# Kernel tuning notes

Measured on AMD Instinct MI355X. Metric: run time of the kernel, lower is better.

Reference implementation:

```python
import jax, jax.numpy as jnp
import numpy as np

HEAD_DIM = 128
N_HEADS = 64
N_KV = 8
N_REP = 8
DIM = 5120
HID = 25600
EPS_LN = 1e-5
EPS_QK = 1e-6
MAX_SEQ = 1024
BSZ = 32


def rmsnorm(x, w, eps):
    xf = x.astype(jnp.float32)
    n = xf * jax.lax.rsqrt(jnp.mean(xf * xf, axis=-1, keepdims=True) + eps)
    return n.astype(x.dtype) * w


def rope(x, cos, sin):
    # x: [b, s, h, d]; cos/sin: [s, d//2]. Complex rotation on (even, odd) pairs.
    xr = x[..., 0::2]
    xi = x[..., 1::2]
    c = cos[None, :, None, :]
    s = sin[None, :, None, :]
    o_r = xr * c - xi * s
    o_i = xr * s + xi * c
    return jnp.stack([o_r, o_i], axis=-1).reshape(x.shape)


def setup_inputs() -> dict:
    key = jax.random.key(0)
    ks = jax.random.split(key, 12)
    seqlen = 1
    start_pos = MAX_SEQ - seqlen
    x = jax.random.normal(ks[0], (BSZ, seqlen, DIM), jnp.float32)
    pos = np.arange(start_pos, start_pos + seqlen)
    inv = 1.0 / (10000.0 ** (np.arange(0, HEAD_DIM, 2, dtype=np.float64) / HEAD_DIM))
    ang = pos[:, None] * inv[None, :]
    freqs_cos = jnp.asarray(np.cos(ang), jnp.float32)
    freqs_sin = jnp.asarray(np.sin(ang), jnp.float32)
    mask = jnp.zeros((1, 1, seqlen, start_pos + seqlen), jnp.float32)
    cache_k = jax.random.normal(ks[1], (BSZ, MAX_SEQ, N_KV, HEAD_DIM), jnp.float32)
    cache_v = jax.random.normal(ks[2], (BSZ, MAX_SEQ, N_KV, HEAD_DIM), jnp.float32)
    s = 0.02
    wq = jax.random.normal(ks[3], (N_HEADS * HEAD_DIM, DIM), jnp.float32) * s
    wk = jax.random.normal(ks[4], (N_KV * HEAD_DIM, DIM), jnp.float32) * s
    wv = jax.random.normal(ks[5], (N_KV * HEAD_DIM, DIM), jnp.float32) * s
    wo = jax.random.normal(ks[6], (DIM, N_HEADS * HEAD_DIM), jnp.float32) * s
    w1 = jax.random.normal(ks[7], (HID, DIM), jnp.float32) * s
    w2 = jax.random.normal(ks[8], (DIM, HID), jnp.float32) * s
    w3 = jax.random.normal(ks[9], (HID, DIM), jnp.float32) * s
    attn_norm_w = jnp.ones((DIM,), jnp.float32)
    ffn_norm_w = jnp.ones((DIM,), jnp.float32)
    q_norm_w = jnp.ones((HEAD_DIM,), jnp.float32)
    k_norm_w = jnp.ones((HEAD_DIM,), jnp.float32)
    return dict(x=x, start_pos=start_pos, freqs_cos=freqs_cos, freqs_sin=freqs_sin,
                mask=mask, cache_k=cache_k, cache_v=cache_v,
                wq=wq, wk=wk, wv=wv, wo=wo, w1=w1, w2=w2, w3=w3,
                attn_norm_w=attn_norm_w, ffn_norm_w=ffn_norm_w,
                q_norm_w=q_norm_w, k_norm_w=k_norm_w)


def reference(x, start_pos, freqs_cos, freqs_sin, mask, cache_k, cache_v,
              wq, wk, wv, wo, w1, w2, w3,
              attn_norm_w, ffn_norm_w, q_norm_w, k_norm_w):
    bsz, seqlen, _ = x.shape
    # --- attention branch ---
    an = rmsnorm(x, attn_norm_w, EPS_LN)
    xq = (an @ wq.T).reshape(bsz, seqlen, N_HEADS, HEAD_DIM)
    xk = (an @ wk.T).reshape(bsz, seqlen, N_KV, HEAD_DIM)
    xv = (an @ wv.T).reshape(bsz, seqlen, N_KV, HEAD_DIM)
    xq = rmsnorm(xq, q_norm_w, EPS_QK)
    xk = rmsnorm(xk, k_norm_w, EPS_QK)
    xq = rope(xq, freqs_cos, freqs_sin)
    xk = rope(xk, freqs_cos, freqs_sin)
    # KV-cache write (start_pos is a static Python int)
    cache_k = cache_k.at[:bsz, start_pos:start_pos + seqlen].set(xk)
    cache_v = cache_v.at[:bsz, start_pos:start_pos + seqlen].set(xv)
    L = start_pos + seqlen
    keys = cache_k[:bsz, :L]      # [b, L, g, d]
    values = cache_v[:bsz, :L]    # [b, L, g, d]
    # GQA via grouped einsum (math-equivalent to repeat_kv then matmul)
    qg = xq.reshape(bsz, seqlen, N_KV, N_REP, HEAD_DIM)  # head = g*N_REP + r
    scores = jnp.einsum('bqgrd,blgd->bgrql', qg, keys) / np.sqrt(HEAD_DIM).astype(np.float32)
    scores = scores + mask[:, :, None, :, :]  # [1,1,1,q,L] broadcast
    probs = jax.nn.softmax(scores.astype(jnp.float32), axis=-1).astype(xq.dtype)
    attn = jnp.einsum('bgrql,blgd->bqgrd', probs, values)
    attn = attn.reshape(bsz, seqlen, N_HEADS * HEAD_DIM)
    h = x + attn @ wo.T
    # --- SwiGLU FFN branch ---
    fn = rmsnorm(h, ffn_norm_w, EPS_LN)
    ff = (jax.nn.silu(fn @ w1.T) * (fn @ w3.T)) @ w2.T
    return h + ff
```

## Files before the change

kernel.cpp:

```cpp
#include <hip/hip_runtime.h>
#include <math.h>

#define DIM   5120
#define QD    8192
#define KVD   1024
#define NQKV  10240
#define NH    64
#define NKV   8
#define HD    128
#define HID   25600
#define SEQL  1024
#define BSZ   32
#define NSEG  8

typedef __attribute__((ext_vector_type(8))) short short8;
typedef __attribute__((ext_vector_type(4))) float f32x4;
typedef __attribute__((ext_vector_type(4))) unsigned short us4;

__device__ __forceinline__ unsigned short f2bf(float f) {
  unsigned u = __builtin_bit_cast(unsigned, f);
  unsigned r = u + 0x7fffu + ((u >> 16) & 1u);
  return (unsigned short)(r >> 16);
}
__device__ __forceinline__ float bf2f(unsigned short b) {
  return __builtin_bit_cast(float, (unsigned)b << 16);
}
__device__ __forceinline__ unsigned cvt2(float lo, float hi) {
  unsigned r;
  asm("v_cvt_pk_bf16_f32 %0, %1, %2" : "=v"(r) : "v"(lo), "v"(hi));
  return r;
}
__device__ __forceinline__ short8 cvt8(float4 a, float4 b) {
  union { unsigned u[4]; short8 s; } o;
  o.u[0] = cvt2(a.x, a.y);
  o.u[1] = cvt2(a.z, a.w);
  o.u[2] = cvt2(b.x, b.y);
  o.u[3] = cvt2(b.z, b.w);
  return o.s;
}
__device__ __forceinline__ float fma4(float4 a, float4 b, float acc) {
  acc = fmaf(a.x, b.x, acc);
  acc = fmaf(a.y, b.y, acc);
  acc = fmaf(a.z, b.z, acc);
  acc = fmaf(a.w, b.w, acc);
  return acc;
}

__global__ __launch_bounds__(256) void rmsnorm_bf_kernel(
    const float* __restrict__ x, const float* __restrict__ w,
    unsigned short* __restrict__ out, float eps) {
  int b = blockIdx.x, t = threadIdx.x;
  const float4* xp = reinterpret_cast<const float4*>(x + (size_t)b * DIM);
  const float4* wp = reinterpret_cast<const float4*>(w);
  us4* op = reinterpret_cast<us4*>(out + (size_t)b * DIM);
  float4 v[5];
  float ss = 0.f;
#pragma unroll
  for (int j = 0; j < 5; ++j) {
    v[j] = xp[t + j * 256];
    ss = fma4(v[j], v[j], ss);
  }
#pragma unroll
  for (int m = 1; m < 64; m <<= 1) ss += __shfl_xor(ss, m);
  __shared__ float red[4];
  if ((t & 63) == 0) red[t >> 6] = ss;
  __syncthreads();
  float sc = rsqrtf((red[0] + red[1] + red[2] + red[3]) * (1.f / DIM) + eps);
#pragma unroll
  for (int j = 0; j < 5; ++j) {
    float4 wv = wp[t + j * 256];
    us4 o;
    o[0] = f2bf(v[j].x * sc * wv.x);
    o[1] = f2bf(v[j].y * sc * wv.y);
    o[2] = f2bf(v[j].z * sc * wv.z);
    o[3] = f2bf(v[j].w * sc * wv.w);
    op[t + j * 256] = o;
  }
}

template <int OUT_BF>
__device__ __forceinline__ void gemm_body(
    const unsigned short* __restrict__ Abf, const float* __restrict__ W,
    void* __restrict__ outp, int K, int k0, int kLen,
    int n0row, int n0col, int Nstride, int t) {
  const int wid = t >> 6, lane = t & 63;
  const int r = lane & 15, kg = lane >> 4;
  const float* wp = W + (size_t)(n0row + wid * 16 + r) * K + k0 + kg * 8;
  const unsigned short* ap0 = Abf + (size_t)r * K + k0 + kg * 8;
  const unsigned short* ap1 = ap0 + (size_t)16 * K;
  f32x4 acc0 = {0.f, 0.f, 0.f, 0.f}, acc1 = {0.f, 0.f, 0.f, 0.f};
#pragma unroll 2
  for (int kk = 0; kk < kLen; kk += 64) {
    float4 w00 = *reinterpret_cast<const float4*>(wp);
    float4 w01 = *reinterpret_cast<const float4*>(wp + 4);
    float4 w10 = *reinterpret_cast<const float4*>(wp + 32);
    float4 w11 = *reinterpret_cast<const float4*>(wp + 36);
    short8 a00 = *reinterpret_cast<const short8*>(ap0);
    short8 a01 = *reinterpret_cast<const short8*>(ap0 + 32);
    short8 a10 = *reinterpret_cast<const short8*>(ap1);
    short8 a11 = *reinterpret_cast<const short8*>(ap1 + 32);
    short8 wf0 = cvt8(w00, w01);
    short8 wf1 = cvt8(w10, w11);
    acc0 = __builtin_amdgcn_mfma_f32_16x16x32_bf16(wf0, a00, acc0, 0, 0, 0);
    acc1 = __builtin_amdgcn_mfma_f32_16x16x32_bf16(wf0, a10, acc1, 0, 0, 0);
    acc0 = __builtin_amdgcn_mfma_f32_16x16x32_bf16(wf1, a01, acc0, 0, 0, 0);
    acc1 = __builtin_amdgcn_mfma_f32_16x16x32_bf16(wf1, a11, acc1, 0, 0, 0);
    wp += 64; ap0 += 64; ap1 += 64;
  }
  int ncol = n0col + wid * 16 + kg * 4;
#pragma unroll
  for (int j = 0; j < 4; ++j) {
    if (OUT_BF) {
      unsigned short* o = (unsigned short*)outp;
      o[(size_t)r * Nstride + ncol + j] = f2bf(acc0[j]);
      o[(size_t)(r + 16) * Nstride + ncol + j] = f2bf(acc1[j]);
    } else {
      float* o = (float*)outp;
      o[(size_t)r * Nstride + ncol + j] = acc0[j];
      o[(size_t)(r + 16) * Nstride + ncol + j] = acc1[j];
    }
  }
}

__global__ __launch_bounds__(128) void qkv_gemm_kernel(
    const unsigned short* __restrict__ an_bf, const float* __restrict__ wq,
    const float* __restrict__ wk, const float* __restrict__ wv,
    float* __restrict__ part) {
  int n = blockIdx.x * 32;
  const float* W;
  int n0row;
  if (n < QD)            { W = wq; n0row = n; }
  else if (n < QD + KVD) { W = wk; n0row = n - QD; }
  else                   { W = wv; n0row = n - QD - KVD; }
  float* outp = part + (size_t)blockIdx.y * BSZ * NQKV;
  gemm_body<0>(an_bf, W, outp, DIM, blockIdx.y * 1280, 1280, n0row, n, NQKV,
               threadIdx.x);
}

__global__ __launch_bounds__(128) void wo_gemm_kernel(
    const unsigned short* __restrict__ ao_bf, const float* __restrict__ wo,
    float* __restrict__ part) {
  int n = blockIdx.x * 32;
  float* outp = part + (size_t)blockIdx.y * BSZ * DIM;
  gemm_body<0>(ao_bf, wo, outp, QD, blockIdx.y * 1024, 1024, n, n, DIM,
               threadIdx.x);
}

__global__ __launch_bounds__(128) void w13_gemm_kernel(
    const unsigned short* __restrict__ fn_bf, const float* __restrict__ w1,
    const float* __restrict__ w3, unsigned short* __restrict__ g13) {
  int n = blockIdx.x * 32;
  const float* W;
  int n0row;
  if (n < HID) { W = w1; n0row = n; }
  else         { W = w3; n0row = n - HID; }
  gemm_body<1>(fn_bf, W, g13, DIM, 0, DIM, n0row, n, 2 * HID, threadIdx.x);
}

__global__ __launch_bounds__(128) void w2_gemm_kernel(
    const unsigned short* __restrict__ gg_bf, const float* __restrict__ w2,
    float* __restrict__ part) {
  int n = blockIdx.x * 32;
  float* outp = part + (size_t)blockIdx.y * BSZ * DIM;
  gemm_body<0>(gg_bf, w2, outp, HID, blockIdx.y * 3200, 3200, n, n, DIM,
               threadIdx.x);
}

__global__ __launch_bounds__(64) void qkv_finish_kernel(
    const float* __restrict__ part, const float* __restrict__ qw,
    const float* __restrict__ kw, const float* __restrict__ fcos,
    const float* __restrict__ fsin, float* __restrict__ xqkv) {
  int h = blockIdx.x, b = blockIdx.y, j = threadIdx.x;
  int base;
  const float* w = nullptr;
  int dorope = 1;
  if (h < NH)            { base = h * HD; w = qw; }
  else if (h < NH + NKV) { base = QD + (h - NH) * HD; w = kw; }
  else                   { base = QD + KVD + (h - NH - NKV) * HD; dorope = 0; }
  size_t off = (size_t)b * NQKV + base;
  float s0 = 0.f, s1 = 0.f;
#pragma unroll
  for (int g = 0; g < 4; ++g) {
    const float* p = part + (size_t)g * BSZ * NQKV + off;
    s0 += p[2 * j];
    s1 += p[2 * j + 1];
  }
  if (dorope) {
    float ss = s0 * s0 + s1 * s1;
#pragma unroll
    for (int m = 1; m < 64; m <<= 1) ss += __shfl_xor(ss, m);
    float sc = rsqrtf(ss * (1.f / HD) + 1e-6f);
    float n0 = s0 * sc * w[2 * j];
    float n1 = s1 * sc * w[2 * j + 1];
    float c = fcos[j], s = fsin[j];
    xqkv[off + 2 * j]     = n0 * c - n1 * s;
    xqkv[off + 2 * j + 1] = n0 * s + n1 * c;
  } else {
    xqkv[off + 2 * j]     = s0;
    xqkv[off + 2 * j + 1] = s1;
  }
}

__global__ __launch_bounds__(256) void wo_finish_kernel(
    const float* __restrict__ part, const float* __restrict__ x,
    const float* __restrict__ fw, float* __restrict__ h,
    unsigned short* __restrict__ fn_bf, float eps) {
  int b = blockIdx.x, t = threadIdx.x;
  const float4* xp = reinterpret_cast<const float4*>(x + (size_t)b * DIM);
  const float4* wp = reinterpret_cast<const float4*>(fw);
  float4* hp = reinterpret_cast<float4*>(h + (size_t)b * DIM);
  us4* fp = reinterpret_cast<us4*>(fn_bf + (size_t)b * DIM);
  float4 v[5];
  float ss = 0.f;
#pragma unroll
  for (int j = 0; j < 5; ++j) {
    int idx = t + j * 256;
    float4 s = xp[idx];
#pragma unroll
    for (int g = 0; g < 8; ++g) {
      float4 p = reinterpret_cast<const float4*>(
          part + (size_t)g * BSZ * DIM + (size_t)b * DIM)[idx];
      s.x += p.x; s.y += p.y; s.z += p.z; s.w += p.w;
    }
    v[j] = s;
    ss = fma4(s, s, ss);
    hp[idx] = s;
  }
#pragma unroll
  for (int m = 1; m < 64; m <<= 1) ss += __shfl_xor(ss, m);
  __shared__ float red[4];
  if ((t & 63) == 0) red[t >> 6] = ss;
  __syncthreads();
  float sc = rsqrtf((red[0] + red[1] + red[2] + red[3]) * (1.f / DIM) + eps);
#pragma unroll
  for (int j = 0; j < 5; ++j) {
    float4 wv = wp[t + j * 256];
    us4 o;
    o[0] = f2bf(v[j].x * sc * wv.x);
    o[1] = f2bf(v[j].y * sc * wv.y);
    o[2] = f2bf(v[j].z * sc * wv.z);
    o[3] = f2bf(v[j].w * sc * wv.w);
    fp[t + j * 256] = o;
  }
}

template <int SEGS>
__global__ __launch_bounds__(256) void combine_kernel(
    const float* __restrict__ part, const float* __restrict__ resid,
    float* __restrict__ out, int total) {
  int i = blockIdx.x * 256 + threadIdx.x;
  if (i >= total) return;
  float s = 0.f;
#pragma unroll
  for (int g = 0; g < SEGS; ++g) s += part[(size_t)g * total + i];
  if (resid) s += resid[i];
  out[i] = s;
}

__global__ __launch_bounds__(256) void attn_kernel(
    const float* __restrict__ xqkv, const float* __restrict__ ck,
    const float* __restrict__ cv, float* __restrict__ pacc,
    float* __restrict__ pml) {
  int g = blockIdx.x, b = blockIdx.y, z = blockIdx.z, t = threadIdx.x;
  __shared__ float qs[8][128];
  __shared__ float tk[128][33];
  __shared__ float tv[32][132];
  __shared__ float st[8][32];
  __shared__ float m_s[8], sum_s[8], fac_s[8];
  const float* qbase = xqkv + (size_t)b * NQKV;
  for (int i = t; i < 8 * 128; i += 256)
    qs[i >> 7][i & 127] = qbase[(g * 8 + (i >> 7)) * HD + (i & 127)];
  if (t < 8) { m_s[t] = -1e30f; sum_s[t] = 0.f; }
  int r = t >> 5, d5 = t & 31;
  float4 acc = make_float4(0.f, 0.f, 0.f, 0.f);
  for (int ti = 0; ti < 1024 / NSEG / 32; ++ti) {
    int l0 = z * (1024 / NSEG) + ti * 32;
    __syncthreads();
#pragma unroll
    for (int jj = 0; jj < 4; ++jj) {
      int i = t + jj * 256;
      int l = i >> 5, d4 = i & 31;
      int gl = l0 + l;
      float4 kv, vv;
      if (gl == 1023) {
        kv = *reinterpret_cast<const float4*>(qbase + QD + g * HD + d4 * 4);
        vv = *reinterpret_cast<const float4*>(qbase + QD + KVD + g * HD + d4 * 4);
      } else {
        size_t base = (((size_t)b * SEQL + gl) * NKV + g) * HD + d4 * 4;
        kv = *reinterpret_cast<const float4*>(ck + base);
        vv = *reinterpret_cast<const float4*>(cv + base);
      }
      tk[d4 * 4 + 0][l] = kv.x;
      tk[d4 * 4 + 1][l] = kv.y;
      tk[d4 * 4 + 2][l] = kv.z;
      tk[d4 * 4 + 3][l] = kv.w;
      *reinterpret_cast<float4*>(&tv[l][d4 * 4]) = vv;
    }
    __syncthreads();
    {
      int l = t & 31, rr = t >> 5;
      float s = 0.f;
#pragma unroll 8
      for (int d = 0; d < 128; ++d) s = fmaf(qs[rr][d], tk[d][l], s);
      st[rr][l] = s * 0.08838834764831845f;
    }
    __syncthreads();
    {
      float sv = st[r][d5];
      float tm = sv;
#pragma unroll
      for (int m = 1; m < 32; m <<= 1) tm = fmaxf(tm, __shfl_xor(tm, m));
      float mo = m_s[r];
      float mn = fmaxf(mo, tm);
      float fac = __expf(mo - mn);
      float e = __expf(sv - mn);
      st[r][d5] = e;
      float ps = e;
#pragma unroll
      for (int m = 1; m < 32; m <<= 1) ps += __shfl_xor(ps, m);
      if (d5 == 0) {
        sum_s[r] = sum_s[r] * fac + ps;
        m_s[r] = mn;
        fac_s[r] = fac;
      }
    }
    __syncthreads();
    {
      float fac = fac_s[r];
      acc.x *= fac; acc.y *= fac; acc.z *= fac; acc.w *= fac;
#pragma unroll 4
      for (int l = 0; l < 32; ++l) {
        float p = st[r][l];
        float4 vv = *reinterpret_cast<const float4*>(&tv[l][d5 * 4]);
        acc.x = fmaf(p, vv.x, acc.x);
        acc.y = fmaf(p, vv.y, acc.y);
        acc.z = fmaf(p, vv.z, acc.z);
        acc.w = fmaf(p, vv.w, acc.w);
      }
    }
  }
  size_t idx = ((size_t)b * NH + g * 8 + r) * NSEG + z;
  *reinterpret_cast<float4*>(pacc + idx * HD + d5 * 4) = acc;
  if (d5 == 0) {
    pml[idx * 2]     = m_s[r];
    pml[idx * 2 + 1] = sum_s[r];
  }
}

__global__ __launch_bounds__(128) void attn_combine_kernel(
    const float* __restrict__ pacc, const float* __restrict__ pml,
    unsigned short* __restrict__ ao_bf) {
  int h = blockIdx.x, b = blockIdx.y, d = threadIdx.x;
  size_t base = ((size_t)b * NH + h) * NSEG;
  float M = -1e30f;
#pragma unroll
  for (int s = 0; s < NSEG; ++s) M = fmaxf(M, pml[(base + s) * 2]);
  float L = 0.f, o = 0.f;
#pragma unroll
  for (int s = 0; s < NSEG; ++s) {
    float w = __expf(pml[(base + s) * 2] - M);
    L += pml[(base + s) * 2 + 1] * w;
    o += pacc[(base + s) * HD + d] * w;
  }
  ao_bf[((size_t)b * NH + h) * HD + d] = f2bf(o / L);
}

__global__ __launch_bounds__(256) void silu_mul_bf_kernel(
    const unsigned short* __restrict__ g13, unsigned short* __restrict__ gg) {
  int j = blockIdx.x * 256 + threadIdx.x;
  int b = blockIdx.y;
  float a = bf2f(g13[(size_t)b * 2 * HID + j]);
  float c = bf2f(g13[(size_t)b * 2 * HID + HID + j]);
  gg[(size_t)b * HID + j] = f2bf((a / (1.f + __expf(-a))) * c);
}

extern "C" void kernel_launch(void* const* d_in, const int* in_sizes, int n_in,
                              void* d_out, int out_size, void* d_ws, size_t ws_size,
                              hipStream_t stream) {
  const float* x    = (const float*)d_in[0];
  const float* fcos = (const float*)d_in[2];
  const float* fsin = (const float*)d_in[3];
  const float* ck   = (const float*)d_in[5];
  const float* cv   = (const float*)d_in[6];
  const float* wq   = (const float*)d_in[7];
  const float* wk   = (const float*)d_in[8];
  const float* wv   = (const float*)d_in[9];
  const float* wo   = (const float*)d_in[10];
  const float* w1   = (const float*)d_in[11];
  const float* w2   = (const float*)d_in[12];
  const float* w3   = (const float*)d_in[13];
  const float* anw  = (const float*)d_in[14];
  const float* fnw  = (const float*)d_in[15];
  const float* qnw  = (const float*)d_in[16];
  const float* knw  = (const float*)d_in[17];
  float* out = (float*)d_out;

  char* wsb = (char*)d_ws;
  float* scratch = (float*)wsb;                 wsb += 16 * 1024 * 1024;
  unsigned short* an_bf  = (unsigned short*)wsb; wsb += (size_t)BSZ * DIM * 2;
  unsigned short* ao_bf  = (unsigned short*)wsb; wsb += (size_t)BSZ * QD * 2;
  unsigned short* g13_bf = (unsigned short*)wsb; wsb += (size_t)BSZ * 2 * HID * 2;
  unsigned short* gg_bf  = (unsigned short*)wsb; wsb += (size_t)BSZ * HID * 2;
  unsigned short* fn_bf  = (unsigned short*)wsb; wsb += (size_t)BSZ * DIM * 2;
  float*          xqkv   = (float*)wsb;          wsb += (size_t)BSZ * NQKV * 4;
  float*          h      = (float*)wsb;          wsb += (size_t)BSZ * DIM * 4;
  float* pacc = scratch;
  float* pml  = scratch + (size_t)BSZ * NH * NSEG * HD;

  rmsnorm_bf_kernel<<<BSZ, 256, 0, stream>>>(x, anw, an_bf, 1e-5f);
  qkv_gemm_kernel<<<dim3(NQKV / 32, 4), 128, 0, stream>>>(an_bf, wq, wk, wv, scratch);
  qkv_finish_kernel<<<dim3(NH + 2 * NKV, BSZ), 64, 0, stream>>>(
      scratch, qnw, knw, fcos, fsin, xqkv);
  attn_kernel<<<dim3(NKV, BSZ, NSEG), 256, 0, stream>>>(xqkv, ck, cv, pacc, pml);
  attn_combine_kernel<<<dim3(NH, BSZ), 128, 0, stream>>>(pacc, pml, ao_bf);
  wo_gemm_kernel<<<dim3(DIM / 32, 8), 128, 0, stream>>>(ao_bf, wo, scratch);
  wo_finish_kernel<<<BSZ, 256, 0, stream>>>(scratch, x, fnw, h, fn_bf, 1e-5f);
  w13_gemm_kernel<<<dim3(2 * HID / 32, 1), 128, 0, stream>>>(fn_bf, w1, w3, g13_bf);
  silu_mul_bf_kernel<<<dim3(HID / 256, BSZ), 256, 0, stream>>>(g13_bf, gg_bf);
  w2_gemm_kernel<<<dim3(DIM / 32, 8), 128, 0, stream>>>(gg_bf, w2, scratch);
  combine_kernel<8><<<(BSZ * DIM + 255) / 256, 256, 0, stream>>>(
      scratch, h, out, BSZ * DIM);
}
```

Before: 658.9 us.

## Stage weight tiles through LDS with coalesced prefetched loads in GEMMs

Rewrites the shared GEMM body so a 256-thread block cooperatively loads a 32-row by 128-column fp32 weight tile with coalesced float4 reads. It converts the tile to bf16 into padded LDS and prefetches the next tile into registers. Each of four waves then computes one 16x16 output tile from LDS-resident weights and global activations. The aim is better DRAM access patterns for the weight-streaming GEMMs, at the cost of two block barriers per k-step and fewer outstanding loads per thread.

```diff
diff --git a/kernel.cpp b/kernel.cpp
--- a/kernel.cpp
+++ b/kernel.cpp
@@ -25,19 +25,6 @@
 __device__ __forceinline__ float bf2f(unsigned short b) {
   return __builtin_bit_cast(float, (unsigned)b << 16);
 }
-__device__ __forceinline__ unsigned cvt2(float lo, float hi) {
-  unsigned r;
-  asm("v_cvt_pk_bf16_f32 %0, %1, %2" : "=v"(r) : "v"(lo), "v"(hi));
-  return r;
-}
-__device__ __forceinline__ short8 cvt8(float4 a, float4 b) {
-  union { unsigned u[4]; short8 s; } o;
-  o.u[0] = cvt2(a.x, a.y);
-  o.u[1] = cvt2(a.z, a.w);
-  o.u[2] = cvt2(b.x, b.y);
-  o.u[3] = cvt2(b.z, b.w);
-  return o.s;
-}
 __device__ __forceinline__ float fma4(float4 a, float4 b, float acc) {
   acc = fmaf(a.x, b.x, acc);
   acc = fmaf(a.y, b.y, acc);
@@ -78,51 +65,68 @@
   }
 }
 
+#define LDSW 136
 template <int OUT_BF>
 __device__ __forceinline__ void gemm_body(
     const unsigned short* __restrict__ Abf, const float* __restrict__ W,
     void* __restrict__ outp, int K, int k0, int kLen,
     int n0row, int n0col, int Nstride, int t) {
-  const int wid = t >> 6, lane = t & 63;
+  __shared__ unsigned short lw[32 * LDSW];
+  const int lane = t & 63;
   const int r = lane & 15, kg = lane >> 4;
-  const float* wp = W + (size_t)(n0row + wid * 16 + r) * K + k0 + kg * 8;
-  const unsigned short* ap0 = Abf + (size_t)r * K + k0 + kg * 8;
-  const unsigned short* ap1 = ap0 + (size_t)16 * K;
-  f32x4 acc0 = {0.f, 0.f, 0.f, 0.f}, acc1 = {0.f, 0.f, 0.f, 0.f};
-#pragma unroll 2
-  for (int kk = 0; kk < kLen; kk += 64) {
-    float4 w00 = *reinterpret_cast<const float4*>(wp);
-    float4 w01 = *reinterpret_cast<const float4*>(wp + 4);
-    float4 w10 = *reinterpret_cast<const float4*>(wp + 32);
-    float4 w11 = *reinterpret_cast<const float4*>(wp + 36);
-    short8 a00 = *reinterpret_cast<const short8*>(ap0);
-    short8 a01 = *reinterpret_cast<const short8*>(ap0 + 32);
-    short8 a10 = *reinterpret_cast<const short8*>(ap1);
-    short8 a11 = *reinterpret_cast<const short8*>(ap1 + 32);
-    short8 wf0 = cvt8(w00, w01);
-    short8 wf1 = cvt8(w10, w11);
-    acc0 = __builtin_amdgcn_mfma_f32_16x16x32_bf16(wf0, a00, acc0, 0, 0, 0);
-    acc1 = __builtin_amdgcn_mfma_f32_16x16x32_bf16(wf0, a10, acc1, 0, 0, 0);
-    acc0 = __builtin_amdgcn_mfma_f32_16x16x32_bf16(wf1, a01, acc0, 0, 0, 0);
-    acc1 = __builtin_amdgcn_mfma_f32_16x16x32_bf16(wf1, a11, acc1, 0, 0, 0);
-    wp += 64; ap0 += 64; ap1 += 64;
-  }
-  int ncol = n0col + wid * 16 + kg * 4;
+  const int wid = t >> 6;
+  const int rgrp = wid & 1, bgrp = wid >> 1;
+  const int srow = t >> 5;
+  const int skf  = (t & 31) * 4;
+  const float* wbase = W + (size_t)n0row * K + k0 + skf;
+  const unsigned short* abase =
+      Abf + (size_t)(bgrp * 16 + r) * K + k0 + kg * 8;
+  f32x4 acc = {0.f, 0.f, 0.f, 0.f};
+  const int nsteps = kLen >> 7;
+  float4 pre[4];
+#pragma unroll
+  for (int j = 0; j < 4; ++j)
+    pre[j] = *reinterpret_cast<const float4*>(wbase + (size_t)(j * 8 + srow) * K);
+  for (int s = 0; s < nsteps; ++s) {
+    __syncthreads();
+#pragma unroll
+    for (int j = 0; j < 4; ++j) {
+      us4 o;
+      o[0] = f2bf(pre[j].x);
+      o[1] = f2bf(pre[j].y);
+      o[2] = f2bf(pre[j].z);
+      o[3] = f2bf(pre[j].w);
+      *reinterpret_cast<us4*>(&lw[(j * 8 + srow) * LDSW + skf]) = o;
+    }
+    if (s + 1 < nsteps) {
+      const float* wb2 = wbase + (size_t)(s + 1) * 128;
+#pragma unroll
+      for (int j = 0; j < 4; ++j)
+        pre[j] = *reinterpret_cast<const float4*>(wb2 + (size_t)(j * 8 + srow) * K);
+    }
+    __syncthreads();
+    const unsigned short* ab = abase + (size_t)s * 128;
+#pragma unroll
+    for (int c = 0; c < 4; ++c) {
+      short8 wf = *reinterpret_cast<const short8*>(
+          &lw[(rgrp * 16 + r) * LDSW + c * 32 + kg * 8]);
+      short8 af = *reinterpret_cast<const short8*>(ab + c * 32);
+      acc = __builtin_amdgcn_mfma_f32_16x16x32_bf16(wf, af, acc, 0, 0, 0);
+    }
+  }
+  int ncol = n0col + rgrp * 16 + kg * 4;
+  int brow = bgrp * 16 + r;
 #pragma unroll
   for (int j = 0; j < 4; ++j) {
     if (OUT_BF) {
-      unsigned short* o = (unsigned short*)outp;
-      o[(size_t)r * Nstride + ncol + j] = f2bf(acc0[j]);
-      o[(size_t)(r + 16) * Nstride + ncol + j] = f2bf(acc1[j]);
+      ((unsigned short*)outp)[(size_t)brow * Nstride + ncol + j] = f2bf(acc[j]);
     } else {
-      float* o = (float*)outp;
-      o[(size_t)r * Nstride + ncol + j] = acc0[j];
-      o[(size_t)(r + 16) * Nstride + ncol + j] = acc1[j];
-    }
-  }
-}
-
-__global__ __launch_bounds__(128) void qkv_gemm_kernel(
+      ((float*)outp)[(size_t)brow * Nstride + ncol + j] = acc[j];
+    }
+  }
+}
+
+__global__ __launch_bounds__(256) void qkv_gemm_kernel(
     const unsigned short* __restrict__ an_bf, const float* __restrict__ wq,
     const float* __restrict__ wk, const float* __restrict__ wv,
     float* __restrict__ part) {
@@ -137,7 +141,7 @@
                threadIdx.x);
 }
 
-__global__ __launch_bounds__(128) void wo_gemm_kernel(
+__global__ __launch_bounds__(256) void wo_gemm_kernel(
     const unsigned short* __restrict__ ao_bf, const float* __restrict__ wo,
     float* __restrict__ part) {
   int n = blockIdx.x * 32;
@@ -146,7 +150,7 @@
                threadIdx.x);
 }
 
-__global__ __launch_bounds__(128) void w13_gemm_kernel(
+__global__ __launch_bounds__(256) void w13_gemm_kernel(
     const unsigned short* __restrict__ fn_bf, const float* __restrict__ w1,
     const float* __restrict__ w3, unsigned short* __restrict__ g13) {
   int n = blockIdx.x * 32;
@@ -157,7 +161,7 @@
   gemm_body<1>(fn_bf, W, g13, DIM, 0, DIM, n0row, n, 2 * HID, threadIdx.x);
 }
 
-__global__ __launch_bounds__(128) void w2_gemm_kernel(
+__global__ __launch_bounds__(256) void w2_gemm_kernel(
     const unsigned short* __restrict__ gg_bf, const float* __restrict__ w2,
     float* __restrict__ part) {
   int n = blockIdx.x * 32;
@@ -408,16 +412,16 @@
   float* pml  = scratch + (size_t)BSZ * NH * NSEG * HD;
 
   rmsnorm_bf_kernel<<<BSZ, 256, 0, stream>>>(x, anw, an_bf, 1e-5f);
-  qkv_gemm_kernel<<<dim3(NQKV / 32, 4), 128, 0, stream>>>(an_bf, wq, wk, wv, scratch);
+  qkv_gemm_kernel<<<dim3(NQKV / 32, 4), 256, 0, stream>>>(an_bf, wq, wk, wv, scratch);
   qkv_finish_kernel<<<dim3(NH + 2 * NKV, BSZ), 64, 0, stream>>>(
       scratch, qnw, knw, fcos, fsin, xqkv);
   attn_kernel<<<dim3(NKV, BSZ, NSEG), 256, 0, stream>>>(xqkv, ck, cv, pacc, pml);
   attn_combine_kernel<<<dim3(NH, BSZ), 128, 0, stream>>>(pacc, pml, ao_bf);
-  wo_gemm_kernel<<<dim3(DIM / 32, 8), 128, 0, stream>>>(ao_bf, wo, scratch);
+  wo_gemm_kernel<<<dim3(DIM / 32, 8), 256, 0, stream>>>(ao_bf, wo, scratch);
   wo_finish_kernel<<<BSZ, 256, 0, stream>>>(scratch, x, fnw, h, fn_bf, 1e-5f);
-  w13_gemm_kernel<<<dim3(2 * HID / 32, 1), 128, 0, stream>>>(fn_bf, w1, w3, g13_bf);
+  w13_gemm_kernel<<<dim3(2 * HID / 32, 1), 256, 0, stream>>>(fn_bf, w1, w3, g13_bf);
   silu_mul_bf_kernel<<<dim3(HID / 256, BSZ), 256, 0, stream>>>(g13_bf, gg_bf);
-  w2_gemm_kernel<<<dim3(DIM / 32, 8), 128, 0, stream>>>(gg_bf, w2, scratch);
+  w2_gemm_kernel<<<dim3(DIM / 32, 8), 256, 0, stream>>>(gg_bf, w2, scratch);
   combine_kernel<8><<<(BSZ * DIM + 255) / 256, 256, 0, stream>>>(
       scratch, h, out, BSZ * DIM);
 }
```

After: 533.0 us. -19.1%, faster.
